# Kernel tuning notes

Hardware: AMD Instinct MI355X
Metric: run time of the kernel (lower is better)

Reference implementation:

```python
import jax, jax.numpy as jnp
import numpy as np

E, H, B, S = 512, 8, 8, 1024  # embed_dim, n_head, batch, n_agent (sequence)
DH = E // H
DECAY_SCALING = 1.0


def _rmsnorm(x, scale, eps=1e-6):
    return x * jax.lax.rsqrt(jnp.mean(x * x, axis=-1, keepdims=True) + eps) * scale


def _groupnorm(y, scale, bias, n_head, eps=1e-5):
    # GroupNorm with num_groups = n_head over the feature axis (flax semantics).
    b, s, e = y.shape
    yg = y.reshape(b, s, n_head, e // n_head)
    mu = jnp.mean(yg, axis=-1, keepdims=True)
    var = jnp.var(yg, axis=-1, keepdims=True)
    yn = (yg - mu) * jax.lax.rsqrt(var + eps)
    return yn.reshape(b, s, e) * scale + bias


def _decay_kappas(n_head, scaling):
    # RetNet multi-scale decays: 1 - exp(linspace(log(1/32), log(1/512), H))
    k = 1.0 - jnp.exp(jnp.linspace(jnp.log(1.0 / 32.0), jnp.log(1.0 / 512.0), n_head))
    return (k * scaling).astype(jnp.float32)


def _msr(key_x, query_x, value_x, wq, wk, wv, wg, wo, gs, gb, kappas):
    # Parallel multi-scale retention (masked / causal, full_self_retention=False).
    b, s, e = query_x.shape
    h = wq.shape[0]
    q = jnp.einsum('bse,hed->bhsd', query_x, wq)
    k = jnp.einsum('bse,hed->bhsd', key_x, wk)
    v = jnp.einsum('bse,hed->bhsd', value_x, wv)
    n = jnp.arange(s)
    diff = n[:, None] - n[None, :]
    causal = diff >= 0
    expnt = jnp.where(causal, diff, 0).astype(q.dtype)
    # D[h,n,m] = kappa_h^(n-m) for n>=m else 0
    D = jnp.where(causal[None], kappas[:, None, None] ** expnt[None], 0.0)
    scores = jnp.einsum('bhnd,bhmd->bhnm', q, k) * D[None]  # [B,H,S,S]
    ret = jnp.einsum('bhnm,bhmd->bhnd', scores, v)
    ret = ret.transpose(0, 2, 1, 3).reshape(b, s, e)
    ret = _groupnorm(ret, gs, gb, h)
    return (jax.nn.swish(query_x @ wg) * ret) @ wo


def _swiglu(x, w_gate, w_lin, w_out):
    return (jax.nn.swish(x @ w_gate) * (x @ w_lin)) @ w_out


def setup_inputs() -> dict:
    key = jax.random.key(0)
    ks = jax.random.split(key, 20)
    sc = 0.02
    d = {
        'x': jax.random.normal(ks[0], (B, S, E), jnp.float32),
        'obs_rep': jax.random.normal(ks[1], (B, S, E), jnp.float32),
        # retention 1 params
        'wq1': jax.random.normal(ks[2], (H, E, DH), jnp.float32) * sc,
        'wk1': jax.random.normal(ks[3], (H, E, DH), jnp.float32) * sc,
        'wv1': jax.random.normal(ks[4], (H, E, DH), jnp.float32) * sc,
        'wg1': jax.random.normal(ks[5], (E, E), jnp.float32) * sc,
        'wo1': jax.random.normal(ks[6], (E, E), jnp.float32) * sc,
        'gs1': jnp.ones((E,), jnp.float32),
        'gb1': jnp.zeros((E,), jnp.float32),
        # retention 2 params
        'wq2': jax.random.normal(ks[7], (H, E, DH), jnp.float32) * sc,
        'wk2': jax.random.normal(ks[8], (H, E, DH), jnp.float32) * sc,
        'wv2': jax.random.normal(ks[9], (H, E, DH), jnp.float32) * sc,
        'wg2': jax.random.normal(ks[10], (E, E), jnp.float32) * sc,
        'wo2': jax.random.normal(ks[11], (E, E), jnp.float32) * sc,
        'gs2': jnp.ones((E,), jnp.float32),
        'gb2': jnp.zeros((E,), jnp.float32),
        # RMSNorm scales
        'ln1_s': jnp.ones((E,), jnp.float32),
        'ln2_s': jnp.ones((E,), jnp.float32),
        'ln3_s': jnp.ones((E,), jnp.float32),
        # SwiGLU(hidden=E, input=E)
        'ffn_w_lin': jax.random.normal(ks[12], (E, E), jnp.float32) * sc,
        'ffn_w_gate': jax.random.normal(ks[13], (E, E), jnp.float32) * sc,
        'ffn_w_out': jax.random.normal(ks[14], (E, E), jnp.float32) * sc,
    }
    return d


def reference(x, obs_rep, wq1, wk1, wv1, wg1, wo1, gs1, gb1,
              wq2, wk2, wv2, wg2, wo2, gs2, gb2,
              ln1_s, ln2_s, ln3_s, ffn_w_lin, ffn_w_gate, ffn_w_out):
    kappas = _decay_kappas(H, DECAY_SCALING)
    # x = ln1(x + retn1(key=x, query=x, value=x))
    x1 = _rmsnorm(x + _msr(x, x, x, wq1, wk1, wv1, wg1, wo1, gs1, gb1, kappas), ln1_s)
    # x = ln2(obs_rep + retn2(key=x1, query=obs_rep, value=x1))
    x2 = _rmsnorm(obs_rep + _msr(x1, obs_rep, x1, wq2, wk2, wv2, wg2, wo2, gs2, gb2, kappas), ln2_s)
    # out = ln3(x2 + ffn(x2))
    return _rmsnorm(x2 + _swiglu(x2, ffn_w_gate, ffn_w_lin, ffn_w_out), ln3_s)
```

## Files before the change

kernel.cpp:

```cpp
#include <hip/hip_runtime.h>
#include <hip/hip_bf16.h>
#include <stdint.h>

typedef unsigned short u16;
typedef unsigned int   u32;
typedef __bf16 bf16x8 __attribute__((ext_vector_type(8)));
typedef u16    u16x8  __attribute__((ext_vector_type(8)));
typedef float  f32x4  __attribute__((ext_vector_type(4)));

#define E_   512
#define H_   8
#define DH_  64
#define B_   8
#define S_   1024
#define M_   (B_ * S_)
#define NTOT (M_ * E_)

__device__ __forceinline__ u16 f2bf(float f) {
    u32 x = __float_as_uint(f);
    x += 0x7fffu + ((x >> 16) & 1u);
    return (u16)(x >> 16);
}
__device__ __forceinline__ float bf2f(u16 b) { return __uint_as_float((u32)b << 16); }
__device__ __forceinline__ bf16x8 as_bf(u16x8 v) {
    union { u16x8 u; bf16x8 b; } x; x.u = v; return x.b;
}
__device__ __forceinline__ u32 cvtpk(float lo, float hi) {
    u32 r;
    asm("v_cvt_pk_bf16_f32 %0, %1, %2" : "=v"(r) : "v"(lo), "v"(hi));
    return r;
}
__device__ __forceinline__ void gll16(const u16* g, u16* l) {
    __builtin_amdgcn_global_load_lds((const __attribute__((address_space(1))) u32*)g,
                                     (__attribute__((address_space(3))) u32*)l, 16, 0, 0);
}
__device__ __forceinline__ void xcd_map(int f, int nwg, int gx, int& bx, int& by) {
    int nf = (f & 7) * (nwg >> 3) + (f >> 3);
    bx = nf % gx; by = nf / gx;
}

__global__ __launch_bounds__(256) void prep_weights(
    const float* __restrict__ wq1, const float* __restrict__ wk1, const float* __restrict__ wv1,
    const float* __restrict__ wg1, const float* __restrict__ wq2, const float* __restrict__ wk2,
    const float* __restrict__ wv2, const float* __restrict__ wg2, const float* __restrict__ wgat,
    const float* __restrict__ wlin, const float* __restrict__ wo1, const float* __restrict__ wo2,
    const float* __restrict__ wout,
    u16* __restrict__ WC1, u16* __restrict__ WC2, u16* __restrict__ WF,
    u16* __restrict__ WO1t, u16* __restrict__ WO2t, u16* __restrict__ WOUt) {
    __shared__ float tle[64][65];
    const int rt = blockIdx.y, c0 = blockIdx.x * 64, tid = threadIdx.x;
    u16* dst; const float* src; int lr0; bool qkv = false; int nb0 = 0, h = 0;
    if (rt < 64) {
        bool s1 = rt < 32;
        dst = s1 ? WC1 : WC2;
        int r = (rt & 31) * 64; lr0 = r;
        if (r < 1536) {
            qkv = true; h = (r >> 6) & 7;
            src = (r < 512) ? (s1 ? wq1 : wq2) : (r < 1024) ? (s1 ? wk1 : wk2) : (s1 ? wv1 : wv2);
        } else { src = s1 ? wg1 : wg2; nb0 = r - 1536; }
    } else if (rt < 80) {
        dst = WF; int r = (rt - 64) * 64; lr0 = r;
        src = (r < 512) ? wgat : wlin; nb0 = r & 511;
    } else if (rt < 88) { dst = WO1t; lr0 = (rt - 80) * 64; src = wo1; nb0 = lr0; }
    else if (rt < 96)   { dst = WO2t; lr0 = (rt - 88) * 64; src = wo2; nb0 = lr0; }
    else                { dst = WOUt; lr0 = (rt - 96) * 64; src = wout; nb0 = lr0; }

    #pragma unroll
    for (int i = 0; i < 16; ++i) {
        int idx = i * 256 + tid, a = idx >> 6, b = idx & 63;
        tle[a][b] = qkv ? src[(size_t)(h * 512 + c0 + a) * 64 + b]
                        : src[(size_t)(c0 + a) * 512 + nb0 + b];
    }
    __syncthreads();
    #pragma unroll
    for (int i = 0; i < 16; ++i) {
        int idx = i * 256 + tid;
        dst[(size_t)(lr0 + (idx >> 6)) * 512 + c0 + (idx & 63)] = f2bf(tle[idx & 63][idx >> 6]);
    }
}

__global__ __launch_bounds__(256) void cvt_both(const float* __restrict__ x,
                                                const float* __restrict__ obs,
                                                u16* __restrict__ XB, u16* __restrict__ OB) {
    int i = blockIdx.x * 256 + threadIdx.x;
    float4 v = ((const float4*)x)[i];
    ushort4 o;
    o.x = f2bf(v.x); o.y = f2bf(v.y); o.z = f2bf(v.z); o.w = f2bf(v.w);
    ((ushort4*)XB)[i] = o;
    v = ((const float4*)obs)[i];
    o.x = f2bf(v.x); o.y = f2bf(v.y); o.z = f2bf(v.z); o.w = f2bf(v.w);
    ((ushort4*)OB)[i] = o;
}

__global__ __launch_bounds__(256) void gemm_qkvg(const u16* __restrict__ A1,
                                                 const u16* __restrict__ A2,
                                                 const u16* __restrict__ W,
                                                 u16* __restrict__ QB, u16* __restrict__ KB,
                                                 u16* __restrict__ KT, u16* __restrict__ VT,
                                                 u16* __restrict__ GB) {
    __shared__ u16 sh[32768];
    const int tid = threadIdx.x;
    const int l = tid & 63, w = tid >> 6;
    const int wm = w & 1, wn = w >> 1;
    int bx, by; xcd_map(blockIdx.x, 1024, 16, bx, by);
    const int bm = by * 128, bn = bx * 128;
    const int which = bx >> 2;
    const u16* A = (which == 1 || which == 2) ? A2 : A1;

    size_t srcA[4], srcB[4]; int ldst[4];
    #pragma unroll
    for (int c = 0; c < 4; ++c) {
        int row = c * 32 + w * 8 + (l >> 3);
        int chs = (l & 7) ^ (row & 7);
        srcA[c] = (size_t)(bm + row) * E_ + chs * 8;
        srcB[c] = (size_t)(bn + row) * E_ + chs * 8;
        ldst[c] = c * 2048 + w * 512;
    }
    int aoff[2][4], boff[2][4];
    #pragma unroll
    for (int kk = 0; kk < 2; ++kk)
        #pragma unroll
        for (int f = 0; f < 4; ++f) {
            int ra = wm * 64 + f * 16 + (l & 15);
            int rb = wn * 64 + f * 16 + (l & 15);
            int ch = kk * 4 + (l >> 4);
            aoff[kk][f] = ra * 128 + ((ch ^ (ra & 7)) << 4);
            boff[kk][f] = rb * 128 + ((ch ^ (rb & 7)) << 4);
        }

    f32x4 acc[4][4] = {};
    #pragma unroll
    for (int c = 0; c < 4; ++c) {
        gll16(A + srcA[c], &sh[ldst[c]]);
        gll16(W + srcB[c], &sh[16384 + ldst[c]]);
    }

    for (int t = 0; t < 8; ++t) {
        const int cur = t & 1;
        if (t < 7) {
            const int k1 = (t + 1) * 64;
            const int nb = (cur ^ 1) * 8192;
            #pragma unroll
            for (int c = 0; c < 4; ++c) {
                gll16(A + srcA[c] + k1, &sh[nb + ldst[c]]);
                gll16(W + srcB[c] + k1, &sh[16384 + nb + ldst[c]]);
            }
            asm volatile("s_waitcnt vmcnt(8)" ::: "memory");
        } else {
            asm volatile("s_waitcnt vmcnt(0)" ::: "memory");
        }
        __builtin_amdgcn_sched_barrier(0);
        __builtin_amdgcn_s_barrier();

        const char* ab = (const char*)sh + cur * 16384;
        const char* bb = (const char*)sh + 32768 + cur * 16384;
        #pragma unroll
        for (int kk = 0; kk < 2; ++kk) {
            bf16x8 af[4], bfr[4];
            #pragma unroll
            for (int f = 0; f < 4; ++f) {
                af[f]  = as_bf(*(const u16x8*)(ab + aoff[kk][f]));
                bfr[f] = as_bf(*(const u16x8*)(bb + boff[kk][f]));
            }
            __builtin_amdgcn_s_setprio(1);
            #pragma unroll
            for (int m = 0; m < 4; ++m)
                #pragma unroll
                for (int n = 0; n < 4; ++n)
                    acc[m][n] = __builtin_amdgcn_mfma_f32_16x16x32_bf16(af[m], bfr[n], acc[m][n], 0, 0, 0);
            __builtin_amdgcn_s_setprio(0);
        }
        if (t < 7) {
            __builtin_amdgcn_s_barrier();
            __builtin_amdgcn_sched_barrier(0);
        }
    }

    if (which != 2) {
        u16* dst = (which == 0) ? QB : (which == 1) ? KB : GB;
        #pragma unroll
        for (int m = 0; m < 4; ++m) {
            int row = bm + wm * 64 + m * 16 + ((l >> 4) << 2);
            #pragma unroll
            for (int n = 0; n < 4; ++n) {
                int coll = (bn & 511) + wn * 64 + n * 16 + (l & 15);
                f32x4 v = acc[m][n];
                #pragma unroll
                for (int r = 0; r < 4; ++r) dst[(size_t)(row + r) * E_ + coll] = f2bf(v[r]);
            }
        }
    }
    if (which == 1 || which == 2) {
        u16* dstT = (which == 2) ? VT : KT;
        __syncthreads();
        #pragma unroll
        for (int m = 0; m < 4; ++m) {
            int row0 = wm * 64 + m * 16 + ((l >> 4) << 2);
            #pragma unroll
            for (int n = 0; n < 4; ++n) {
                int c = wn * 64 + n * 16 + (l & 15);
                f32x4 v = acc[m][n];
                uint2 pk; pk.x = cvtpk(v[0], v[1]); pk.y = cvtpk(v[2], v[3]);
                int off = c * 256 + (((row0 >> 3) ^ (c & 7)) << 4) + ((row0 & 7) << 1);
                *(uint2*)((char*)sh + off) = pk;
            }
        }
        __syncthreads();
        int c = tid >> 1, half = tid & 1;
        int collg = (bn & 511) + c;
        int bh = ((bm >> 10) << 3) + (collg >> 6);
        size_t gb = ((size_t)bh * 64 + (collg & 63)) * 1024 + (bm & 1023) + half * 64;
        #pragma unroll
        for (int j = 0; j < 8; ++j) {
            int chunk = half * 8 + j;
            uint4 vv = *(const uint4*)((const char*)sh + c * 256 + ((chunk ^ (c & 7)) << 4));
            *(uint4*)(dstT + gb + j * 8) = vv;
        }
    }
}

__global__ __launch_bounds__(256) void state_u(const u16* __restrict__ KT,
                                               const u16* __restrict__ VT,
                                               u16* __restrict__ U) {
    const int id = blockIdx.x;
    const int bh = id >> 3, c = id & 7;
    const int h = bh & 7;
    const int l = threadIdx.x & 63, w = threadIdx.x >> 6;
    const float kappa = 1.0f - __expf(-3.46573590f + (float)h * -0.39608410f);
    const float log2k = log2f(kappa);
    const float ik = 1.0f / kappa;

    bf16x8 af[4];
    {
        size_t vbase = ((size_t)bh * 64 + (w * 16 + (l & 15))) * 1024 + c * 128 + ((l >> 4) << 3);
        #pragma unroll
        for (int kk = 0; kk < 4; ++kk)
            af[kk] = as_bf(*(const u16x8*)(VT + vbase + kk * 32));
    }

    f32x4 acc[4] = {};
    #pragma unroll
    for (int fd = 0; fd < 4; ++fd) {
        size_t kbase = ((size_t)bh * 64 + (fd * 16 + (l & 15))) * 1024 + c * 128 + ((l >> 4) << 3);
        #pragma unroll
        for (int kk = 0; kk < 4; ++kk) {
            u16x8 kv = *(const u16x8*)(KT + kbase + kk * 32);
            int mb = kk * 32 + ((l >> 4) << 3);
            float wj = exp2f((float)(127 - mb) * log2k);
            u16x8 kw;
            #pragma unroll
            for (int j = 0; j < 8; ++j) { kw[j] = f2bf(bf2f(kv[j]) * wj); wj *= ik; }
            acc[fd] = __builtin_amdgcn_mfma_f32_16x16x32_bf16(af[kk], as_bf(kw), acc[fd], 0, 0, 0);
        }
    }

    #pragma unroll
    for (int fd = 0; fd < 4; ++fd) {
        int dv = w * 16 + ((l >> 4) << 2);
        int dk = fd * 16 + (l & 15);
        size_t ub = ((size_t)id * 64 + dv) * 64 + dk;
        #pragma unroll
        for (int r = 0; r < 4; ++r) U[ub + (size_t)r * 64] = f2bf(acc[fd][r]);
    }
}

__global__ __launch_bounds__(256) void retention_chunk(
        const u16* __restrict__ Q, const u16* __restrict__ K,
        const u16* __restrict__ VT, const u16* __restrict__ U,
        const u16* __restrict__ G,
        const float* __restrict__ gs, const float* __restrict__ gb,
        u16* __restrict__ T) {
    __shared__ u16 Ks[128 * 64], Vts[64 * 128], Ps[128 * 64], Ss[64 * 64];
    const int tid = threadIdx.x;
    const int l = tid & 63, w = tid >> 6;
    const int id = blockIdx.x;
    const int bh = id >> 3, c = id & 7;
    const int h = bh & 7;
    const int n0 = c * 128;
    const size_t base = (size_t)(bh >> 3) * (S_ * E_) + h * DH_;

    const float kappa = 1.0f - __expf(-3.46573590f + (float)h * -0.39608410f);
    const float log2k = log2f(kappa);
    const float ik = 1.0f / kappa;
    const float ikp2 = ik * ik, ikp3 = ikp2 * ik;

    float gsv[4], gbv[4];
    #pragma unroll
    for (int fd = 0; fd < 4; ++fd) {
        gsv[fd] = gs[h * 64 + fd * 16 + (l & 15)];
        gbv[fd] = gb[h * 64 + fd * 16 + (l & 15)];
    }

    #pragma unroll
    for (int cc = 0; cc < 4; ++cc) {
        int row = cc * 32 + w * 8 + (l >> 3);
        int chs = (l & 7) ^ (row & 7);
        gll16(K + base + (size_t)(n0 + row) * E_ + chs * 8, &Ks[cc * 2048 + w * 512]);
        int d = cc * 16 + w * 4 + (l >> 4);
        int vch = (l & 15) ^ (d & 15);
        gll16(VT + ((size_t)bh * 64 + d) * 1024 + n0 + vch * 8, &Vts[cc * 2048 + w * 512]);
    }

    bf16x8 qf[2][2];
    #pragma unroll
    for (int kk = 0; kk < 2; ++kk)
        #pragma unroll
        for (int fn = 0; fn < 2; ++fn) {
            int n = n0 + fn * 64 + w * 16 + (l & 15);
            qf[kk][fn] = as_bf(*(const u16x8*)(Q + base + (size_t)n * E_ + kk * 32 + ((l >> 4) << 3)));
        }

    if (c > 0) {
        float accs[16];
        #pragma unroll
        for (int j = 0; j < 16; ++j) accs[j] = 0.f;
        const float kC = exp2f(128.0f * log2k);
        float wc = 1.0f;
        size_t ub = (size_t)bh * (8 * 4096) + tid * 16;
        for (int cp = c - 1; cp >= 0; --cp) {
            const u16* up = U + ub + (size_t)cp * 4096;
            u16x8 a = *(const u16x8*)up;
            u16x8 b = *(const u16x8*)(up + 8);
            #pragma unroll
            for (int j = 0; j < 8; ++j) {
                accs[j]     += bf2f(a[j]) * wc;
                accs[8 + j] += bf2f(b[j]) * wc;
            }
            wc *= kC;
        }
        int dv = tid >> 2, ch0 = (tid & 3) << 1;
        #pragma unroll
        for (int hh = 0; hh < 2; ++hh) {
            uint4 pk;
            pk.x = cvtpk(accs[hh * 8 + 0], accs[hh * 8 + 1]);
            pk.y = cvtpk(accs[hh * 8 + 2], accs[hh * 8 + 3]);
            pk.z = cvtpk(accs[hh * 8 + 4], accs[hh * 8 + 5]);
            pk.w = cvtpk(accs[hh * 8 + 6], accs[hh * 8 + 7]);
            *(uint4*)((char*)Ss + dv * 128 + (((ch0 + hh) ^ (dv & 7)) << 4)) = pk;
        }
    }
    __syncthreads();

    f32x4 acc[2][4] = {};

    if (c > 0) {
        __builtin_amdgcn_s_setprio(1);
        #pragma unroll
        for (int kk = 0; kk < 2; ++kk) {
            bf16x8 sf[4];
            #pragma unroll
            for (int fd = 0; fd < 4; ++fd) {
                int dv = fd * 16 + (l & 15);
                int ch = kk * 4 + (l >> 4);
                sf[fd] = as_bf(*(const u16x8*)((const char*)Ss + dv * 128 + ((ch ^ (dv & 7)) << 4)));
            }
            #pragma unroll
            for (int fn = 0; fn < 2; ++fn)
                #pragma unroll
                for (int fd = 0; fd < 4; ++fd)
                    acc[fn][fd] = __builtin_amdgcn_mfma_f32_16x16x32_bf16(qf[kk][fn], sf[fd], acc[fn][fd], 0, 0, 0);
        }
        __builtin_amdgcn_s_setprio(0);
        #pragma unroll
        for (int fn = 0; fn < 2; ++fn) {
            int nl0 = fn * 64 + w * 16 + ((l >> 4) << 2);
            float fr0 = exp2f((float)(nl0 + 1) * log2k);
            float fr1 = fr0 * kappa, fr2 = fr1 * kappa, fr3 = fr2 * kappa;
            #pragma unroll
            for (int fd = 0; fd < 4; ++fd) {
                acc[fn][fd][0] *= fr0; acc[fn][fd][1] *= fr1;
                acc[fn][fd][2] *= fr2; acc[fn][fd][3] *= fr3;
            }
        }
    }

    #pragma unroll
    for (int mh = 0; mh < 2; ++mh) {
        const int m0l = mh * 64;
        bf16x8 kf[2][4];
        #pragma unroll
        for (int kk = 0; kk < 2; ++kk)
            #pragma unroll
            for (int f = 0; f < 4; ++f) {
                int row = m0l + f * 16 + (l & 15);
                int ch = kk * 4 + (l >> 4);
                kf[kk][f] = as_bf(*(const u16x8*)((const char*)Ks + row * 128 + ((ch ^ (row & 7)) << 4)));
            }
        #pragma unroll
        for (int fn = 0; fn < 2; ++fn) {
            if (mh == 1 && fn == 0) continue;
            f32x4 s[4] = {};
            __builtin_amdgcn_s_setprio(1);
            #pragma unroll
            for (int kk = 0; kk < 2; ++kk)
                #pragma unroll
                for (int f = 0; f < 4; ++f)
                    s[f] = __builtin_amdgcn_mfma_f32_16x16x32_bf16(kf[kk][f], qf[kk][fn], s[f], 0, 0, 0);
            __builtin_amdgcn_s_setprio(0);
            const bool fast = (mh == 0 && fn == 1);
            int nl = fn * 64 + w * 16 + (l & 15);
            #pragma unroll
            for (int f = 0; f < 4; ++f) {
                int mbl = m0l + f * 16 + ((l >> 4) << 2);
                int delta = nl - mbl;
                float wb = exp2f((float)delta * log2k);
                f32x4 v = s[f];
                float p0, p1, p2, p3;
                if (fast) {
                    float w1 = wb * ik, w2 = w1 * ik, w3 = w2 * ik;
                    p0 = v[0] * wb; p1 = v[1] * w1; p2 = v[2] * w2; p3 = v[3] * w3;
                } else {
                    p0 = (delta >= 0) ? v[0] * wb : 0.f;
                    p1 = (delta >= 1) ? v[1] * wb * ik : 0.f;
                    p2 = (delta >= 2) ? v[2] * wb * ikp2 : 0.f;
                    p3 = (delta >= 3) ? v[3] * wb * ikp3 : 0.f;
                }
                int mcl = f * 16 + ((l >> 4) << 2);
                int byteoff = nl * 128 + (((mcl >> 3) ^ (nl & 7)) << 4) + ((mcl & 4) << 1);
                uint2 pk;
                pk.x = cvtpk(p0, p1);
                pk.y = cvtpk(p2, p3);
                *(uint2*)((char*)Ps + byteoff) = pk;
            }
        }
        #pragma unroll
        for (int km = 0; km < 2; ++km) {
            bf16x8 pf[2];
            #pragma unroll
            for (int fn = 0; fn < 2; ++fn) {
                if (mh == 1 && fn == 0) continue;
                int row = fn * 64 + w * 16 + (l & 15);
                int ch = km * 4 + (l >> 4);
                pf[fn] = as_bf(*(const u16x8*)((const char*)Ps + row * 128 + ((ch ^ (row & 7)) << 4)));
            }
            __builtin_amdgcn_s_setprio(1);
            #pragma unroll
            for (int fd = 0; fd < 4; ++fd) {
                int d = fd * 16 + (l & 15);
                int mch = mh * 8 + km * 4 + (l >> 4);
                bf16x8 vfr = as_bf(*(const u16x8*)((const char*)Vts + d * 256 + ((mch ^ (d & 15)) << 4)));
                #pragma unroll
                for (int fn = 0; fn < 2; ++fn) {
                    if (mh == 1 && fn == 0) continue;
                    acc[fn][fd] = __builtin_amdgcn_mfma_f32_16x16x32_bf16(pf[fn], vfr, acc[fn][fd], 0, 0, 0);
                }
            }
            __builtin_amdgcn_s_setprio(0);
        }
    }

    #pragma unroll
    for (int fn = 0; fn < 2; ++fn) {
        #pragma unroll
        for (int r = 0; r < 4; ++r) {
            float s1 = 0.f, s2 = 0.f;
            #pragma unroll
            for (int fd = 0; fd < 4; ++fd) { float v = acc[fn][fd][r]; s1 += v; s2 += v * v; }
            #pragma unroll
            for (int off = 1; off < 16; off <<= 1) {
                s1 += __shfl_xor(s1, off, 64);
                s2 += __shfl_xor(s2, off, 64);
            }
            float mean = s1 * (1.f / 64.f);
            float var  = s2 * (1.f / 64.f) - mean * mean;
            float rinv = rsqrtf(var + 1e-5f);
            int rowg = n0 + fn * 64 + w * 16 + ((l >> 4) << 2) + r;
            size_t rb = base + (size_t)rowg * E_;
            #pragma unroll
            for (int fd = 0; fd < 4; ++fd) {
                int d = fd * 16 + (l & 15);
                float ny = (acc[fn][fd][r] - mean) * rinv;
                float rn = ny * gsv[fd] + gbv[fd];
                float g = bf2f(G[rb + d]);
                T[rb + d] = f2bf(g * rn / (1.f + __expf(-g)));
            }
        }
    }
}

__global__ __launch_bounds__(256) void gemm_wo(const u16* __restrict__ A,
                                               const u16* __restrict__ W,
                                               u16* __restrict__ Cb) {
    __shared__ u16 sh[24576];
    const int tid = threadIdx.x;
    const int l = tid & 63, w = tid >> 6;
    const int wm = w & 1, wn = w >> 1;
    int bx, by; xcd_map(blockIdx.x, 512, 4, bx, by);
    const int bm = by * 64, bn = bx * 128;

    size_t srcA[2], srcB[4]; int ldstA[2], ldstB[4];
    #pragma unroll
    for (int c = 0; c < 4; ++c) {
        int row = c * 32 + w * 8 + (l >> 3);
        int chs = (l & 7) ^ (row & 7);
        if (c < 2) { srcA[c] = (size_t)(bm + row) * E_ + chs * 8; ldstA[c] = c * 2048 + w * 512; }
        srcB[c] = (size_t)(bn + row) * E_ + chs * 8;
        ldstB[c] = c * 2048 + w * 512;
    }
    int aoff[2][2], boff[2][4];
    #pragma unroll
    for (int kk = 0; kk < 2; ++kk) {
        #pragma unroll
        for (int f = 0; f < 2; ++f) {
            int ra = wm * 32 + f * 16 + (l & 15);
            aoff[kk][f] = ra * 128 + (((kk * 4 + (l >> 4)) ^ (ra & 7)) << 4);
        }
        #pragma unroll
        for (int f = 0; f < 4; ++f) {
            int rb = wn * 64 + f * 16 + (l & 15);
            boff[kk][f] = rb * 128 + (((kk * 4 + (l >> 4)) ^ (rb & 7)) << 4);
        }
    }

    f32x4 acc[2][4] = {};
    #pragma unroll
    for (int c = 0; c < 2; ++c) gll16(A + srcA[c], &sh[ldstA[c]]);
    #pragma unroll
    for (int c = 0; c < 4; ++c) gll16(W + srcB[c], &sh[8192 + ldstB[c]]);

    for (int t = 0; t < 8; ++t) {
        const int cur = t & 1;
        if (t < 7) {
            const int k1 = (t + 1) * 64;
            const int na = (cur ^ 1) * 4096, nb = (cur ^ 1) * 8192;
            #pragma unroll
            for (int c = 0; c < 2; ++c) gll16(A + srcA[c] + k1, &sh[na + ldstA[c]]);
            #pragma unroll
            for (int c = 0; c < 4; ++c) gll16(W + srcB[c] + k1, &sh[8192 + nb + ldstB[c]]);
            asm volatile("s_waitcnt vmcnt(6)" ::: "memory");
        } else {
            asm volatile("s_waitcnt vmcnt(0)" ::: "memory");
        }
        __builtin_amdgcn_sched_barrier(0);
        __builtin_amdgcn_s_barrier();

        const char* ab = (const char*)sh + cur * 8192;
        const char* bb = (const char*)sh + 16384 + cur * 16384;
        #pragma unroll
        for (int kk = 0; kk < 2; ++kk) {
            bf16x8 af[2], bfr[4];
            #pragma unroll
            for (int f = 0; f < 2; ++f) af[f] = as_bf(*(const u16x8*)(ab + aoff[kk][f]));
            #pragma unroll
            for (int f = 0; f < 4; ++f) bfr[f] = as_bf(*(const u16x8*)(bb + boff[kk][f]));
            __builtin_amdgcn_s_setprio(1);
            #pragma unroll
            for (int m = 0; m < 2; ++m)
                #pragma unroll
                for (int n = 0; n < 4; ++n)
                    acc[m][n] = __builtin_amdgcn_mfma_f32_16x16x32_bf16(af[m], bfr[n], acc[m][n], 0, 0, 0);
            __builtin_amdgcn_s_setprio(0);
        }
        if (t < 7) {
            __builtin_amdgcn_s_barrier();
            __builtin_amdgcn_sched_barrier(0);
        }
    }

    #pragma unroll
    for (int m = 0; m < 2; ++m) {
        int row = bm + wm * 32 + m * 16 + ((l >> 4) << 2);
        #pragma unroll
        for (int n = 0; n < 4; ++n) {
            int col = bn + wn * 64 + n * 16 + (l & 15);
            f32x4 v = acc[m][n];
            #pragma unroll
            for (int r = 0; r < 4; ++r) Cb[(size_t)(row + r) * E_ + col] = f2bf(v[r]);
        }
    }
}

__global__ __launch_bounds__(256) void gemm_ffn(const u16* __restrict__ A,
                                                const u16* __restrict__ W,
                                                u16* __restrict__ T) {
    __shared__ u16 sh[24576];
    const int tid = threadIdx.x;
    const int l = tid & 63, w = tid >> 6;
    const int wm = w & 1, wn = w >> 1;
    int bx, by; xcd_map(blockIdx.x, 1024, 8, bx, by);
    const int bm = by * 64, bn = bx * 64;

    size_t srcA[2], srcG[2], srcL[2]; int ldst[2];
    #pragma unroll
    for (int c = 0; c < 2; ++c) {
        int row = c * 32 + w * 8 + (l >> 3);
        int chs = (l & 7) ^ (row & 7);
        srcA[c] = (size_t)(bm + row) * E_ + chs * 8;
        srcG[c] = (size_t)(bn + row) * E_ + chs * 8;
        srcL[c] = (size_t)(512 + bn + row) * E_ + chs * 8;
        ldst[c] = c * 2048 + w * 512;
    }
    int aoff[2][2], goff[2][2];
    #pragma unroll
    for (int kk = 0; kk < 2; ++kk)
        #pragma unroll
        for (int f = 0; f < 2; ++f) {
            int ra = wm * 32 + f * 16 + (l & 15);
            int rb = wn * 32 + f * 16 + (l & 15);
            aoff[kk][f] = ra * 128 + (((kk * 4 + (l >> 4)) ^ (ra & 7)) << 4);
            goff[kk][f] = rb * 128 + (((kk * 4 + (l >> 4)) ^ (rb & 7)) << 4);
        }

    f32x4 accg[2][2] = {}, accl[2][2] = {};
    #pragma unroll
    for (int c = 0; c < 2; ++c) {
        gll16(A + srcA[c], &sh[ldst[c]]);
        gll16(W + srcG[c], &sh[8192 + ldst[c]]);
        gll16(W + srcL[c], &sh[16384 + ldst[c]]);
    }

    for (int t = 0; t < 8; ++t) {
        const int cur = t & 1;
        if (t < 7) {
            const int k1 = (t + 1) * 64;
            const int nb = (cur ^ 1) * 4096;
            #pragma unroll
            for (int c = 0; c < 2; ++c) {
                gll16(A + srcA[c] + k1, &sh[nb + ldst[c]]);
                gll16(W + srcG[c] + k1, &sh[8192 + nb + ldst[c]]);
                gll16(W + srcL[c] + k1, &sh[16384 + nb + ldst[c]]);
            }
            asm volatile("s_waitcnt vmcnt(6)" ::: "memory");
        } else {
            asm volatile("s_waitcnt vmcnt(0)" ::: "memory");
        }
        __builtin_amdgcn_sched_barrier(0);
        __builtin_amdgcn_s_barrier();

        const char* ab = (const char*)sh + cur * 8192;
        const char* gb = (const char*)sh + 16384 + cur * 8192;
        const char* lb = (const char*)sh + 32768 + cur * 8192;
        #pragma unroll
        for (int kk = 0; kk < 2; ++kk) {
            bf16x8 af[2], bg[2], bl[2];
            #pragma unroll
            for (int f = 0; f < 2; ++f) {
                af[f] = as_bf(*(const u16x8*)(ab + aoff[kk][f]));
                bg[f] = as_bf(*(const u16x8*)(gb + goff[kk][f]));
                bl[f] = as_bf(*(const u16x8*)(lb + goff[kk][f]));
            }
            __builtin_amdgcn_s_setprio(1);
            #pragma unroll
            for (int m = 0; m < 2; ++m)
                #pragma unroll
                for (int n = 0; n < 2; ++n) {
                    accg[m][n] = __builtin_amdgcn_mfma_f32_16x16x32_bf16(af[m], bg[n], accg[m][n], 0, 0, 0);
                    accl[m][n] = __builtin_amdgcn_mfma_f32_16x16x32_bf16(af[m], bl[n], accl[m][n], 0, 0, 0);
                }
            __builtin_amdgcn_s_setprio(0);
        }
        if (t < 7) {
            __builtin_amdgcn_s_barrier();
            __builtin_amdgcn_sched_barrier(0);
        }
    }

    #pragma unroll
    for (int m = 0; m < 2; ++m) {
        int row = bm + wm * 32 + m * 16 + ((l >> 4) << 2);
        #pragma unroll
        for (int n = 0; n < 2; ++n) {
            int col = bn + wn * 32 + n * 16 + (l & 15);
            #pragma unroll
            for (int r = 0; r < 4; ++r) {
                float g = accg[m][n][r], lv = accl[m][n][r];
                T[(size_t)(row + r) * E_ + col] = f2bf(g * lv / (1.f + __expf(-g)));
            }
        }
    }
}

__global__ __launch_bounds__(256) void rmsnorm_res(const u16* __restrict__ Xb,
                                                   const u16* __restrict__ Yb,
                                                   const float* __restrict__ sc,
                                                   float* __restrict__ outf,
                                                   u16* __restrict__ outb) {
    int row = blockIdx.x * 4 + (threadIdx.x >> 6);
    int l = threadIdx.x & 63;
    size_t off = (size_t)row * E_ + l * 8;
    u16x8 xv = *(const u16x8*)(Xb + off);
    u16x8 yv = *(const u16x8*)(Yb + off);
    float v[8]; float sq = 0.f;
    #pragma unroll
    for (int j = 0; j < 8; ++j) { v[j] = bf2f(xv[j]) + bf2f(yv[j]); sq += v[j] * v[j]; }
    #pragma unroll
    for (int o = 1; o < 64; o <<= 1) sq += __shfl_xor(sq, o, 64);
    float rinv = rsqrtf(sq * (1.0f / 512.0f) + 1e-6f);
    float4 s0 = ((const float4*)sc)[l * 2];
    float4 s1 = ((const float4*)sc)[l * 2 + 1];
    float sv[8] = {s0.x, s0.y, s0.z, s0.w, s1.x, s1.y, s1.z, s1.w};
    if (outb) {
        u16x8 o8;
        #pragma unroll
        for (int j = 0; j < 8; ++j) o8[j] = f2bf(v[j] * rinv * sv[j]);
        *(u16x8*)(outb + off) = o8;
    }
    if (outf) {
        float4 o0, o1;
        o0.x = v[0]*rinv*sv[0]; o0.y = v[1]*rinv*sv[1]; o0.z = v[2]*rinv*sv[2]; o0.w = v[3]*rinv*sv[3];
        o1.x = v[4]*rinv*sv[4]; o1.y = v[5]*rinv*sv[5]; o1.z = v[6]*rinv*sv[6]; o1.w = v[7]*rinv*sv[7];
        ((float4*)(outf))[(off >> 2)]     = o0;
        ((float4*)(outf))[(off >> 2) + 1] = o1;
    }
}

extern "C" void kernel_launch(void* const* d_in, const int* in_sizes, int n_in,
                              void* d_out, int out_size, void* d_ws, size_t ws_size,
                              hipStream_t stream) {
    const float* x    = (const float*)d_in[0];
    const float* obs  = (const float*)d_in[1];
    const float* wq1  = (const float*)d_in[2];
    const float* wk1  = (const float*)d_in[3];
    const float* wv1  = (const float*)d_in[4];
    const float* wg1  = (const float*)d_in[5];
    const float* wo1  = (const float*)d_in[6];
    const float* gs1  = (const float*)d_in[7];
    const float* gb1  = (const float*)d_in[8];
    const float* wq2  = (const float*)d_in[9];
    const float* wk2  = (const float*)d_in[10];
    const float* wv2  = (const float*)d_in[11];
    const float* wg2  = (const float*)d_in[12];
    const float* wo2  = (const float*)d_in[13];
    const float* gs2  = (const float*)d_in[14];
    const float* gb2  = (const float*)d_in[15];
    const float* ln1s = (const float*)d_in[16];
    const float* ln2s = (const float*)d_in[17];
    const float* ln3s = (const float*)d_in[18];
    const float* wlin = (const float*)d_in[19];
    const float* wgat = (const float*)d_in[20];
    const float* wout = (const float*)d_in[21];

    u16* wsb = (u16*)d_ws;
    u16* WC1  = wsb;
    u16* WC2  = WC1 + 2048 * 512;
    u16* WF   = WC2 + 2048 * 512;
    u16* WO1t = WF + 1024 * 512;
    u16* WO2t = WO1t + 512 * 512;
    u16* WOUt = WO2t + 512 * 512;
    u16* XB   = WOUt + 512 * 512;
    u16* OB   = XB + NTOT;
    u16* QB   = OB + NTOT;
    u16* KB   = QB + NTOT;
    u16* KT   = KB + NTOT;
    u16* VT   = KT + NTOT;
    u16* GB   = VT + NTOT;
    u16* TB   = GB + NTOT;
    u16* UB   = TB + NTOT;
    u16* YB   = QB;

    dim3 tG(256);

    prep_weights<<<dim3(8, 104), tG, 0, stream>>>(wq1, wk1, wv1, wg1, wq2, wk2, wv2, wg2,
                                                  wgat, wlin, wo1, wo2, wout,
                                                  WC1, WC2, WF, WO1t, WO2t, WOUt);
    cvt_both<<<NTOT / 1024, tG, 0, stream>>>(x, obs, XB, OB);

    gemm_qkvg<<<1024, tG, 0, stream>>>(XB, XB, WC1, QB, KB, KT, VT, GB);
    state_u<<<512, tG, 0, stream>>>(KT, VT, UB);
    retention_chunk<<<512, tG, 0, stream>>>(QB, KB, VT, UB, GB, gs1, gb1, TB);
    gemm_wo<<<512, tG, 0, stream>>>(TB, WO1t, YB);
    rmsnorm_res<<<M_ / 4, tG, 0, stream>>>(XB, YB, ln1s, nullptr, XB);

    gemm_qkvg<<<1024, tG, 0, stream>>>(OB, XB, WC2, QB, KB, KT, VT, GB);
    state_u<<<512, tG, 0, stream>>>(KT, VT, UB);
    retention_chunk<<<512, tG, 0, stream>>>(QB, KB, VT, UB, GB, gs2, gb2, TB);
    gemm_wo<<<512, tG, 0, stream>>>(TB, WO2t, YB);
    rmsnorm_res<<<M_ / 4, tG, 0, stream>>>(OB, YB, ln2s, nullptr, OB);

    gemm_ffn<<<1024, tG, 0, stream>>>(OB, WF, TB);
    gemm_wo<<<512, tG, 0, stream>>>(TB, WOUt, YB);
    rmsnorm_res<<<M_ / 4, tG, 0, stream>>>(OB, YB, ln3s, (float*)d_out, nullptr);
}
```

Before: 170.9 us.

## Enlarge QKVG GEMM tiles to 256x256 with 512-thread blocks

The fused Q/K/V/G projection GEMM moves from 128x128 tiles with 256 threads to 256x256 tiles with 512 threads (8 waves, each computing 128x64). LDS doubles to 128KB, and the grid shrinks from 1024 to 256 blocks. The A-fragment loads are interleaved with the MFMA calls. The goal is more reuse of each loaded tile and less global traffic per FLOP. The costs are one block per CU, only 256 blocks on a GPU with many CUs (possible tail and under-occupancy), and higher register pressure from the 8x4 accumulators.

```diff
diff --git a/kernel.cpp b/kernel.cpp
--- a/kernel.cpp
+++ b/kernel.cpp
@@ -92,58 +92,61 @@
     ((ushort4*)OB)[i] = o;
 }
 
-__global__ __launch_bounds__(256) void gemm_qkvg(const u16* __restrict__ A1,
-                                                 const u16* __restrict__ A2,
-                                                 const u16* __restrict__ W,
-                                                 u16* __restrict__ QB, u16* __restrict__ KB,
-                                                 u16* __restrict__ KT, u16* __restrict__ VT,
-                                                 u16* __restrict__ GB) {
-    __shared__ u16 sh[32768];
+__global__ __launch_bounds__(512, 1) void gemm_qkvg(const u16* __restrict__ A1,
+                                                    const u16* __restrict__ A2,
+                                                    const u16* __restrict__ W,
+                                                    u16* __restrict__ QB, u16* __restrict__ KB,
+                                                    u16* __restrict__ KT, u16* __restrict__ VT,
+                                                    u16* __restrict__ GB) {
+    __shared__ u16 sh[65536];
     const int tid = threadIdx.x;
     const int l = tid & 63, w = tid >> 6;
-    const int wm = w & 1, wn = w >> 1;
-    int bx, by; xcd_map(blockIdx.x, 1024, 16, bx, by);
-    const int bm = by * 128, bn = bx * 128;
-    const int which = bx >> 2;
+    const int wm = w >> 2, wn = w & 3;
+    int bx, by; xcd_map(blockIdx.x, 256, 8, bx, by);
+    const int bm = by * 256, bn = bx * 256;
+    const int which = bx >> 1;
     const u16* A = (which == 1 || which == 2) ? A2 : A1;
 
     size_t srcA[4], srcB[4]; int ldst[4];
     #pragma unroll
     for (int c = 0; c < 4; ++c) {
-        int row = c * 32 + w * 8 + (l >> 3);
+        int row = c * 64 + w * 8 + (l >> 3);
         int chs = (l & 7) ^ (row & 7);
         srcA[c] = (size_t)(bm + row) * E_ + chs * 8;
         srcB[c] = (size_t)(bn + row) * E_ + chs * 8;
-        ldst[c] = c * 2048 + w * 512;
-    }
-    int aoff[2][4], boff[2][4];
-    #pragma unroll
-    for (int kk = 0; kk < 2; ++kk)
+        ldst[c] = c * 4096 + w * 512;
+    }
+    int aoff[2][8], boff[2][4];
+    #pragma unroll
+    for (int kk = 0; kk < 2; ++kk) {
+        #pragma unroll
+        for (int f = 0; f < 8; ++f) {
+            int ra = wm * 128 + f * 16 + (l & 15);
+            aoff[kk][f] = ra * 128 + (((kk * 4 + (l >> 4)) ^ (ra & 7)) << 4);
+        }
         #pragma unroll
         for (int f = 0; f < 4; ++f) {
-            int ra = wm * 64 + f * 16 + (l & 15);
             int rb = wn * 64 + f * 16 + (l & 15);
-            int ch = kk * 4 + (l >> 4);
-            aoff[kk][f] = ra * 128 + ((ch ^ (ra & 7)) << 4);
-            boff[kk][f] = rb * 128 + ((ch ^ (rb & 7)) << 4);
-        }
-
-    f32x4 acc[4][4] = {};
+            boff[kk][f] = rb * 128 + (((kk * 4 + (l >> 4)) ^ (rb & 7)) << 4);
+        }
+    }
+
+    f32x4 acc[8][4] = {};
     #pragma unroll
     for (int c = 0; c < 4; ++c) {
         gll16(A + srcA[c], &sh[ldst[c]]);
-        gll16(W + srcB[c], &sh[16384 + ldst[c]]);
+        gll16(W + srcB[c], &sh[32768 + ldst[c]]);
     }
 
     for (int t = 0; t < 8; ++t) {
         const int cur = t & 1;
         if (t < 7) {
             const int k1 = (t + 1) * 64;
-            const int nb = (cur ^ 1) * 8192;
+            const int nb = (cur ^ 1) * 16384;
             #pragma unroll
             for (int c = 0; c < 4; ++c) {
                 gll16(A + srcA[c] + k1, &sh[nb + ldst[c]]);
-                gll16(W + srcB[c] + k1, &sh[16384 + nb + ldst[c]]);
+                gll16(W + srcB[c] + k1, &sh[32768 + nb + ldst[c]]);
             }
             asm volatile("s_waitcnt vmcnt(8)" ::: "memory");
         } else {
@@ -152,23 +155,22 @@
         __builtin_amdgcn_sched_barrier(0);
         __builtin_amdgcn_s_barrier();
 
-        const char* ab = (const char*)sh + cur * 16384;
-        const char* bb = (const char*)sh + 32768 + cur * 16384;
+        const char* ab = (const char*)sh + cur * 32768;
+        const char* bb = (const char*)sh + 65536 + cur * 32768;
         #pragma unroll
         for (int kk = 0; kk < 2; ++kk) {
-            bf16x8 af[4], bfr[4];
-            #pragma unroll
-            for (int f = 0; f < 4; ++f) {
-                af[f]  = as_bf(*(const u16x8*)(ab + aoff[kk][f]));
-                bfr[f] = as_bf(*(const u16x8*)(bb + boff[kk][f]));
-            }
-            __builtin_amdgcn_s_setprio(1);
-            #pragma unroll
-            for (int m = 0; m < 4; ++m)
+            bf16x8 bfr[4];
+            #pragma unroll
+            for (int f = 0; f < 4; ++f) bfr[f] = as_bf(*(const u16x8*)(bb + boff[kk][f]));
+            #pragma unroll
+            for (int f = 0; f < 8; ++f) {
+                bf16x8 af = as_bf(*(const u16x8*)(ab + aoff[kk][f]));
+                __builtin_amdgcn_s_setprio(1);
                 #pragma unroll
                 for (int n = 0; n < 4; ++n)
-                    acc[m][n] = __builtin_amdgcn_mfma_f32_16x16x32_bf16(af[m], bfr[n], acc[m][n], 0, 0, 0);
-            __builtin_amdgcn_s_setprio(0);
+                    acc[f][n] = __builtin_amdgcn_mfma_f32_16x16x32_bf16(af, bfr[n], acc[f][n], 0, 0, 0);
+                __builtin_amdgcn_s_setprio(0);
+            }
         }
         if (t < 7) {
             __builtin_amdgcn_s_barrier();
@@ -179,12 +181,12 @@
     if (which != 2) {
         u16* dst = (which == 0) ? QB : (which == 1) ? KB : GB;
         #pragma unroll
-        for (int m = 0; m < 4; ++m) {
-            int row = bm + wm * 64 + m * 16 + ((l >> 4) << 2);
+        for (int f = 0; f < 8; ++f) {
+            int row = bm + wm * 128 + f * 16 + ((l >> 4) << 2);
             #pragma unroll
             for (int n = 0; n < 4; ++n) {
-                int coll = (bn & 511) + wn * 64 + n * 16 + (l & 15);
-                f32x4 v = acc[m][n];
+                int coll = (bx & 1) * 256 + wn * 64 + n * 16 + (l & 15);
+                f32x4 v = acc[f][n];
                 #pragma unroll
                 for (int r = 0; r < 4; ++r) dst[(size_t)(row + r) * E_ + coll] = f2bf(v[r]);
             }
@@ -194,26 +196,26 @@
         u16* dstT = (which == 2) ? VT : KT;
         __syncthreads();
         #pragma unroll
-        for (int m = 0; m < 4; ++m) {
-            int row0 = wm * 64 + m * 16 + ((l >> 4) << 2);
+        for (int f = 0; f < 8; ++f) {
+            int row0 = wm * 128 + f * 16 + ((l >> 4) << 2);
             #pragma unroll
             for (int n = 0; n < 4; ++n) {
                 int c = wn * 64 + n * 16 + (l & 15);
-                f32x4 v = acc[m][n];
+                f32x4 v = acc[f][n];
                 uint2 pk; pk.x = cvtpk(v[0], v[1]); pk.y = cvtpk(v[2], v[3]);
-                int off = c * 256 + (((row0 >> 3) ^ (c & 7)) << 4) + ((row0 & 7) << 1);
+                int off = c * 512 + (((row0 >> 3) ^ (c & 7)) << 4) + ((row0 & 7) << 1);
                 *(uint2*)((char*)sh + off) = pk;
             }
         }
         __syncthreads();
-        int c = tid >> 1, half = tid & 1;
-        int collg = (bn & 511) + c;
+        int c2 = tid >> 1, half = tid & 1;
+        int collg = (bx & 1) * 256 + c2;
         int bh = ((bm >> 10) << 3) + (collg >> 6);
-        size_t gb = ((size_t)bh * 64 + (collg & 63)) * 1024 + (bm & 1023) + half * 64;
-        #pragma unroll
-        for (int j = 0; j < 8; ++j) {
-            int chunk = half * 8 + j;
-            uint4 vv = *(const uint4*)((const char*)sh + c * 256 + ((chunk ^ (c & 7)) << 4));
+        size_t gb = ((size_t)bh * 64 + (collg & 63)) * 1024 + (bm & 1023) + half * 128;
+        #pragma unroll
+        for (int j = 0; j < 16; ++j) {
+            int chunk = half * 16 + j;
+            uint4 vv = *(const uint4*)((const char*)sh + c2 * 512 + ((chunk ^ (c2 & 7)) << 4));
             *(uint4*)(dstT + gb + j * 8) = vv;
         }
     }
@@ -755,13 +757,13 @@
                                                   WC1, WC2, WF, WO1t, WO2t, WOUt);
     cvt_both<<<NTOT / 1024, tG, 0, stream>>>(x, obs, XB, OB);
 
-    gemm_qkvg<<<1024, tG, 0, stream>>>(XB, XB, WC1, QB, KB, KT, VT, GB);
+    gemm_qkvg<<<256, 512, 0, stream>>>(XB, XB, WC1, QB, KB, KT, VT, GB);
     state_u<<<512, tG, 0, stream>>>(KT, VT, UB);
     retention_chunk<<<512, tG, 0, stream>>>(QB, KB, VT, UB, GB, gs1, gb1, TB);
     gemm_wo<<<512, tG, 0, stream>>>(TB, WO1t, YB);
     rmsnorm_res<<<M_ / 4, tG, 0, stream>>>(XB, YB, ln1s, nullptr, XB);
 
-    gemm_qkvg<<<1024, tG, 0, stream>>>(OB, XB, WC2, QB, KB, KT, VT, GB);
+    gemm_qkvg<<<256, 512, 0, stream>>>(OB, XB, WC2, QB, KB, KT, VT, GB);
     state_u<<<512, tG, 0, stream>>>(KT, VT, UB);
     retention_chunk<<<512, tG, 0, stream>>>(QB, KB, VT, UB, GB, gs2, gb2, TB);
     gemm_wo<<<512, tG, 0, stream>>>(TB, WO2t, YB);
```

After: 181.2 us. 1.06x slower.
